# Optimization experiments

Measured on AMD Instinct MI355X. Metric: run time of the kernel, lower is better.

The kernel has to match this reference:

```python
import jax, jax.numpy as jnp
import numpy as np

BLOCK = 64      # block_size
NRAND = 3       # num_random_blocks
NUM_HEAD = 16
HEAD_DIM = 64
HIDDEN = 1024
PEN = -10000.0  # HF attn_mask_penalty


def _sparse_attn(q, k, v, band_mask, from_mask, to_mask, blocked_mask, rand_attn):
    # q,k,v: [B,H,S,D]; BigBird block-sparse attention (HF math).
    B, H, S, D = q.shape
    b, r = BLOCK, NRAND
    n = S // b
    rsd = 1.0 / (D ** 0.5)

    bq = q.reshape(B, H, n, b, D)
    bk = k.reshape(B, H, n, b, D)
    bv = v.reshape(B, H, n, b, D)

    bi = jnp.arange(B)[:, None, None, None]
    hi = jnp.arange(H)[None, :, None, None]
    # gathered random key/value blocks: [B,H,n-2,r*b,D]
    gk = bk[bi, hi, rand_attn].reshape(B, H, n - 2, r * b, D)
    gv = bv[bi, hi, rand_attn].reshape(B, H, n - 2, r * b, D)
    # random-block mask: [B,H,n-2,b,r*b]
    rm = blocked_mask[bi, rand_attn].reshape(B, H, n - 2, r * b)
    rand_mask = jnp.einsum("blq,bhlk->bhlqk", blocked_mask[:, 1:-1], rm)

    ones = lambda shp: jnp.ones(shp, q.dtype)

    # ---- first query block: attends to everything ----
    p = jnp.einsum("bhqd,bhkd->bhqk", bq[:, :, 0], k) * rsd + (1.0 - to_mask) * PEN
    c0 = jnp.einsum("bhqk,bhkd->bhqd", jax.nn.softmax(p, -1), v)[:, :, None]

    # ---- second query block: blocks 0,1,2,last + random ----
    k1 = jnp.concatenate([bk[:, :, 0], bk[:, :, 1], bk[:, :, 2], bk[:, :, -1], gk[:, :, 0]], axis=2)
    v1 = jnp.concatenate([bv[:, :, 0], bv[:, :, 1], bv[:, :, 2], bv[:, :, -1], gv[:, :, 0]], axis=2)
    p = jnp.einsum("bhqd,bhkd->bhqk", bq[:, :, 1], k1) * rsd
    seq_pad = jnp.concatenate([to_mask[..., :3 * b], to_mask[..., -b:], ones((B, 1, 1, r * b))], axis=3)
    rand_pad = jnp.concatenate([ones((B, H, b, 4 * b)), rand_mask[:, :, 0]], axis=3)
    p = p + (1.0 - jnp.minimum(seq_pad, rand_pad)) * PEN
    c1 = jnp.einsum("bhqk,bhkd->bhqd", jax.nn.softmax(p, -1), v1)[:, :, None]

    # ---- middle blocks 2..n-3: band(3 blocks) + first + last + random ----
    ek = jnp.concatenate([bk[:, :, 1:-3], bk[:, :, 2:-2], bk[:, :, 3:-1]], axis=3)  # [B,H,n-4,3b,D]
    ev = jnp.concatenate([bv[:, :, 1:-3], bv[:, :, 2:-2], bv[:, :, 3:-1]], axis=3)
    mq = bq[:, :, 2:-2]                                                              # [B,H,n-4,b,D]
    inner = jnp.einsum("bhlqd,bhlkd->bhlqk", mq, ek) * rsd + (1.0 - band_mask) * PEN
    randp = jnp.einsum("bhlqd,bhlkd->bhlqk", mq, gk[:, :, 1:-1]) * rsd + (1.0 - rand_mask[:, :, 1:-1]) * PEN
    firstp = jnp.einsum("bhlqd,bhkd->bhlqk", mq, bk[:, :, 0]) * rsd + (1.0 - to_mask[..., :b][:, :, None]) * PEN
    lastp = jnp.einsum("bhlqd,bhkd->bhlqk", mq, bk[:, :, -1]) * rsd + (1.0 - to_mask[..., -b:][:, :, None]) * PEN
    band = jnp.concatenate([firstp, inner, randp, lastp], axis=-1)  # [B,H,n-4,b,(5+r)*b]
    a = jax.nn.softmax(band, -1)
    cm = jnp.einsum("bhlqk,bhlkd->bhlqd", a[..., b:4 * b], ev)
    cm = cm + jnp.einsum("bhlqk,bhlkd->bhlqd", a[..., 4 * b:-b], gv[:, :, 1:-1])
    cm = cm + jnp.einsum("bhlqk,bhkd->bhlqd", a[..., :b], bv[:, :, 0])
    cm = cm + jnp.einsum("bhlqk,bhkd->bhlqd", a[..., -b:], bv[:, :, -1])

    # ---- second-last query block: blocks 0,-3,-2,-1 + random ----
    k2 = jnp.concatenate([bk[:, :, 0], bk[:, :, -3], bk[:, :, -2], bk[:, :, -1], gk[:, :, -1]], axis=2)
    v2 = jnp.concatenate([bv[:, :, 0], bv[:, :, -3], bv[:, :, -2], bv[:, :, -1], gv[:, :, -1]], axis=2)
    p = jnp.einsum("bhqd,bhkd->bhqk", bq[:, :, -2], k2) * rsd
    seq_pad = jnp.concatenate([to_mask[..., :b], to_mask[..., -3 * b:], ones((B, 1, 1, r * b))], axis=3)
    rand_pad = jnp.concatenate([ones((B, H, b, 4 * b)), rand_mask[:, :, -1]], axis=3)
    p = p + (1.0 - jnp.minimum(seq_pad, rand_pad)) * PEN
    c2 = jnp.einsum("bhqk,bhkd->bhqd", jax.nn.softmax(p, -1), v2)[:, :, None]

    # ---- last query block: attends to everything ----
    p = jnp.einsum("bhqd,bhkd->bhqk", bq[:, :, -1], k) * rsd + (1.0 - to_mask) * PEN
    c3 = jnp.einsum("bhqk,bhkd->bhqd", jax.nn.softmax(p, -1), v)[:, :, None]

    ctx = jnp.concatenate([c0, c1, cm, c2, c3], axis=2).reshape(B, H, S, D)
    ctx = ctx * from_mask  # [B,1,S,1]
    return ctx.transpose(0, 2, 1, 3).reshape(B, S, H * D)


def setup_inputs() -> dict:
    key = jax.random.key(0)
    ks = jax.random.split(key, 12)
    B, L = 2, 4064
    S = 4096
    n = S // BLOCK
    sc = 0.02
    inp = {
        "X": jax.random.normal(ks[0], (B, L, HIDDEN), jnp.float32),
        "Wq": jax.random.normal(ks[1], (HIDDEN, NUM_HEAD * HEAD_DIM), jnp.float32) * sc,
        "b_q": jnp.zeros((NUM_HEAD * HEAD_DIM,), jnp.float32),
        "Wk": jax.random.normal(ks[2], (HIDDEN, NUM_HEAD * HEAD_DIM), jnp.float32) * sc,
        "b_k": jnp.zeros((NUM_HEAD * HEAD_DIM,), jnp.float32),
        "Wv": jax.random.normal(ks[3], (HIDDEN, NUM_HEAD * HEAD_DIM), jnp.float32) * sc,
        "b_v": jnp.zeros((NUM_HEAD * HEAD_DIM,), jnp.float32),
        "Wo": jax.random.normal(ks[4], (NUM_HEAD * HEAD_DIM, HIDDEN), jnp.float32) * sc,
        "b_o": jnp.zeros((HIDDEN,), jnp.float32),
        "band_mask": jnp.ones((B, 1, n - 4, BLOCK, 3 * BLOCK), jnp.float32),
        "from_mask": jnp.ones((B, 1, S, 1), jnp.float32),
        "to_mask": jnp.ones((B, 1, 1, S), jnp.float32),
        "blocked_encoder_mask": jnp.ones((B, n, BLOCK), jnp.float32),
        "rand_attn": jax.random.randint(ks[5], (B, NUM_HEAD, n - 2, NRAND), 0, n, jnp.int32),
    }
    return inp


def reference(X, Wq, b_q, Wk, b_k, Wv, b_v, Wo, b_o,
              band_mask, from_mask, to_mask, blocked_encoder_mask, rand_attn):
    B, L, _ = X.shape
    pad = BLOCK - L % BLOCK  # matches torch wrapper (pads full block if L % b == 0)
    Xp = jnp.pad(X, ((0, 0), (0, pad), (0, 0)))
    S = L + pad

    def proj(W, bias):
        return (Xp @ W + bias).reshape(B, S, NUM_HEAD, HEAD_DIM).transpose(0, 2, 1, 3)

    q, k, v = proj(Wq, b_q), proj(Wk, b_k), proj(Wv, b_v)
    attn = _sparse_attn(q, k, v, band_mask, from_mask, to_mask, blocked_encoder_mask, rand_attn)
    out = attn @ Wo + b_o
    return out[:, :L]
```

## Files before the change

### kernel.cpp

```cpp
#include <hip/hip_runtime.h>

#define BB 2
#define SEQ 4096
#define LQ 4064
#define HID 1024
#define NH 16
#define HD 64
#define NB 64
#define BLK 64
#define NR 3
#define PENV -10000.0f

typedef __bf16 bf16;
typedef __bf16 bf16x8 __attribute__((ext_vector_type(8)));
typedef float floatx4 __attribute__((ext_vector_type(4)));

__device__ inline floatx4 mfma16(bf16x8 a, bf16x8 b, floatx4 c) {
    return __builtin_amdgcn_mfma_f32_16x16x32_bf16(a, b, c, 0, 0, 0);
}

__device__ inline void async_ld16(const bf16* g, bf16* l) {
    __builtin_amdgcn_global_load_lds(
        (const __attribute__((address_space(1))) unsigned int*)g,
        (__attribute__((address_space(3))) unsigned int*)l, 16, 0, 0);
}

__global__ __launch_bounds__(256) void cast_pad_x(const float* __restrict__ X,
                                                  bf16* __restrict__ Xp) {
    int t = blockIdx.x * 256 + threadIdx.x;
    int c4 = t & 255;
    int row = t >> 8;
    int b = row >> 12;
    int s = row & 4095;
    float4 v = make_float4(0.f, 0.f, 0.f, 0.f);
    if (s < LQ) {
        v = reinterpret_cast<const float4*>(X + ((size_t)(b * LQ + s)) * HID)[c4];
    }
    union { bf16 h[4]; uint2 u; } o;
    o.h[0] = (bf16)v.x; o.h[1] = (bf16)v.y; o.h[2] = (bf16)v.z; o.h[3] = (bf16)v.w;
    *reinterpret_cast<uint2*>(Xp + (size_t)row * HID + c4 * 4) = o.u;
}

__global__ __launch_bounds__(256) void transpose_w(const float* __restrict__ Wq,
                                                   const float* __restrict__ Wk,
                                                   const float* __restrict__ Wv,
                                                   const float* __restrict__ Wo,
                                                   bf16* __restrict__ WqkvT,
                                                   bf16* __restrict__ WoT) {
    __shared__ float tile[64][65];
    int sel = blockIdx.z;
    const float* src = (sel == 0) ? Wq : (sel == 1) ? Wk : (sel == 2) ? Wv : Wo;
    bf16* dst = (sel < 3) ? (WqkvT + (size_t)sel * HID * HID) : WoT;
    int j0 = blockIdx.x * 64, k0 = blockIdx.y * 64;
    int tx = threadIdx.x, ty = threadIdx.y;
    for (int i = 0; i < 16; i++) {
        int k = ty + i * 4;
        tile[k][tx] = src[(size_t)(k0 + k) * HID + j0 + tx];
    }
    __syncthreads();
    for (int i = 0; i < 16; i++) {
        int j = ty + i * 4;
        dst[(size_t)(j0 + j) * HID + k0 + tx] = (bf16)tile[tx][j];
    }
}

__global__ __launch_bounds__(256) void transpose_band(const float* __restrict__ band,
                                                      float* __restrict__ bandT) {
    __shared__ float tile[64][65];
    int kt = blockIdx.x;
    int lrow = blockIdx.y;
    int b = blockIdx.z;
    const float* src = band + ((size_t)(b * (NB - 4) + lrow) * BLK) * 192;
    float* dst = bandT + ((size_t)(b * (NB - 4) + lrow) * 192) * BLK;
    int tx = threadIdx.x, ty = threadIdx.y;
    for (int i = 0; i < 16; i++) {
        int qq = i * 4 + ty;
        tile[qq][tx] = src[(size_t)qq * 192 + kt * 64 + tx];
    }
    __syncthreads();
    for (int i = 0; i < 16; i++) {
        int k = i * 4 + ty;
        dst[(size_t)(kt * 64 + k) * BLK + tx] = tile[tx][k];
    }
}

__global__ __launch_bounds__(256) void gemm_qkv(const bf16* __restrict__ Xp,
                                                const bf16* __restrict__ WT,
                                                const float* __restrict__ bq,
                                                const float* __restrict__ bk,
                                                const float* __restrict__ bv,
                                                bf16* __restrict__ qo,
                                                bf16* __restrict__ ko,
                                                bf16* __restrict__ vt) {
    __shared__ __align__(16) bf16 As[128 * 64];
    __shared__ __align__(16) bf16 Bs[128 * 64];
    int tid = threadIdx.x;
    int wave = tid >> 6, lane = tid & 63;
    int quad = lane >> 4, lm = lane & 15;
    int tile_m = blockIdx.x * 128;
    int tile_n = blockIdx.y * 128;
    int wm = (wave & 1) * 64, wn = (wave >> 1) * 64;

    floatx4 acc[4][4] = {};

    for (int k0 = 0; k0 < HID; k0 += 64) {
        __syncthreads();
        for (int it = 0; it < 4; it++) {
            int c = it * 256 + tid;
            int row = c >> 3, col = (c & 7) * 8;
            async_ld16(Xp + (size_t)(tile_m + row) * HID + k0 + col, &As[c * 8]);
            async_ld16(WT + (size_t)(tile_n + row) * HID + k0 + col, &Bs[c * 8]);
        }
        __syncthreads();
        for (int ks = 0; ks < 64; ks += 32) {
            bf16x8 a[4], b[4];
            for (int i = 0; i < 4; i++)
                a[i] = *reinterpret_cast<const bf16x8*>(&As[(wm + i * 16 + lm) * 64 + ks + quad * 8]);
            for (int j = 0; j < 4; j++)
                b[j] = *reinterpret_cast<const bf16x8*>(&Bs[(wn + j * 16 + lm) * 64 + ks + quad * 8]);
            for (int i = 0; i < 4; i++)
                for (int j = 0; j < 4; j++)
                    acc[i][j] = mfma16(a[i], b[j], acc[i][j]);
        }
    }

    for (int i = 0; i < 4; i++) {
        for (int j = 0; j < 4; j++) {
            int nn = tile_n + wn + j * 16 + lm;
            int which = nn >> 10;
            int hc = nn & 1023;
            const float* bias = (which == 0) ? bq : (which == 1) ? bk : bv;
            float bsv = bias[hc];
            int h = hc >> 6, d = hc & 63;
            for (int r = 0; r < 4; r++) {
                int mm = tile_m + wm + i * 16 + quad * 4 + r;
                int b_ = mm >> 12, s = mm & 4095;
                float val = acc[i][j][r] + bsv;
                if (which == 0) {
                    qo[((size_t)((b_ * NH + h) * SEQ + s)) * HD + d] = (bf16)(val * 0.125f);
                } else if (which == 1) {
                    ko[((size_t)((b_ * NH + h) * SEQ + s)) * HD + d] = (bf16)val;
                } else {
                    vt[((size_t)((b_ * NH + h) * HD + d)) * SEQ + s] = (bf16)val;
                }
            }
        }
    }
}

__global__ __launch_bounds__(256, 2) void attn_kernel(const bf16* __restrict__ q,
                                                      const bf16* __restrict__ kk,
                                                      const bf16* __restrict__ vt,
                                                      const float* __restrict__ bandT,
                                                      const float* __restrict__ fromm,
                                                      const float* __restrict__ tom,
                                                      const float* __restrict__ blocked,
                                                      const int* __restrict__ rand_attn,
                                                      bf16* __restrict__ attn) {
    __shared__ __align__(16) char smem[33792 + 512];

    int tid = threadIdx.x, wave = tid >> 6, lane = tid & 63;
    int quad = lane >> 4, lm = lane & 15;
    int bh = blockIdx.x;
    int b = bh >> 4, h = bh & 15;
    size_t bh_base = (size_t)bh * SEQ * HD;
    int x = blockIdx.y;
    bool fullmode = (x < 8);
    int l, sub;
    if (fullmode) { l = (x >> 2) ? (NB - 1) : 0; sub = x & 3; }
    else          { l = x - 7;                   sub = wave;  }

    bf16x8 aq0 = *reinterpret_cast<const bf16x8*>(
        q + bh_base + (size_t)(l * BLK + sub * 16 + lm) * HD + quad * 8);
    bf16x8 aq1 = *reinterpret_cast<const bf16x8*>(
        q + bh_base + (size_t)(l * BLK + sub * 16 + lm) * HD + 32 + quad * 8);

    floatx4 ctx[4] = {};
    float mrun = -1e30f, lrun = 0.f;
    float mq = blocked[((size_t)b * NB + l) * BLK + sub * 16 + lm];

    int blist[8], btype[8];
    if (!fullmode) {
        int base;
        if (l == 1) {
            blist[0] = 0; blist[1] = 1; blist[2] = 2; blist[3] = NB - 1;
            btype[0] = btype[1] = btype[2] = btype[3] = 0;
            base = 4;
        } else if (l == NB - 2) {
            blist[0] = 0; blist[1] = NB - 3; blist[2] = NB - 2; blist[3] = NB - 1;
            btype[0] = btype[1] = btype[2] = btype[3] = 0;
            base = 4;
        } else {
            blist[0] = 0;      btype[0] = 0;
            blist[1] = l - 1;  btype[1] = 1;
            blist[2] = l;      btype[2] = 2;
            blist[3] = l + 1;  btype[3] = 3;
            blist[4] = NB - 1; btype[4] = 0;
            base = 5;
        }
        const int* ra = rand_attn + ((size_t)(b * NH + h) * (NB - 2) + (l - 1)) * NR;
        for (int r = 0; r < NR; r++) { blist[base + r] = ra[r]; btype[base + r] = 4; }
        for (int i = base + NR; i < 8; i++) { blist[i] = 0; btype[i] = 5; }
    }

    bf16* pw = (bf16*)smem + wave * 16 * 264;

    int nch = fullmode ? 4 : 2;
    for (int ch = 0; ch < nch; ch++) {
        floatx4 sc[4][4];
        #pragma unroll
        for (int ib = 0; ib < 4; ib++) {
            int kb  = fullmode ? (wave * 16 + ch * 4 + ib) : blist[ch * 4 + ib];
            int typ = fullmode ? 0 : btype[ch * 4 + ib];
            const bf16* kbase = kk + bh_base + (size_t)kb * BLK * HD;
            #pragma unroll
            for (int f = 0; f < 4; f++) {
                bf16x8 a0 = *reinterpret_cast<const bf16x8*>(kbase + (f * 16 + lm) * HD + quad * 8);
                bf16x8 a1 = *reinterpret_cast<const bf16x8*>(kbase + (f * 16 + lm) * HD + 32 + quad * 8);
                floatx4 z = {0.f, 0.f, 0.f, 0.f};
                z = mfma16(a0, aq0, z);
                z = mfma16(a1, aq1, z);
                sc[ib][f] = z;
            }
            if (typ == 0) {
                #pragma unroll
                for (int f = 0; f < 4; f++) {
                    float4 t4 = *reinterpret_cast<const float4*>(
                        tom + (size_t)b * SEQ + kb * BLK + f * 16 + quad * 4);
                    sc[ib][f][0] += (1.f - t4.x) * PENV;
                    sc[ib][f][1] += (1.f - t4.y) * PENV;
                    sc[ib][f][2] += (1.f - t4.z) * PENV;
                    sc[ib][f][3] += (1.f - t4.w) * PENV;
                }
            } else if (typ == 4) {
                #pragma unroll
                for (int f = 0; f < 4; f++) {
                    float4 t4 = *reinterpret_cast<const float4*>(
                        blocked + ((size_t)b * NB + kb) * BLK + f * 16 + quad * 4);
                    sc[ib][f][0] += (1.f - mq * t4.x) * PENV;
                    sc[ib][f][1] += (1.f - mq * t4.y) * PENV;
                    sc[ib][f][2] += (1.f - mq * t4.z) * PENV;
                    sc[ib][f][3] += (1.f - mq * t4.w) * PENV;
                }
            } else if (typ != 5) {
                int t = typ - 1;
                const float* bp = bandT + ((size_t)(b * (NB - 4) + (l - 2)) * 192 + t * 64) * BLK;
                #pragma unroll
                for (int f = 0; f < 4; f++)
                    #pragma unroll
                    for (int r = 0; r < 4; r++) {
                        float bm = bp[(size_t)(f * 16 + quad * 4 + r) * BLK + sub * 16 + lm];
                        sc[ib][f][r] += (1.f - bm) * PENV;
                    }
            } else {
                #pragma unroll
                for (int f = 0; f < 4; f++)
                    #pragma unroll
                    for (int r = 0; r < 4; r++) sc[ib][f][r] += PENV;
            }
        }

        float mx = -1e30f;
        #pragma unroll
        for (int ib = 0; ib < 4; ib++)
            #pragma unroll
            for (int f = 0; f < 4; f++)
                #pragma unroll
                for (int r = 0; r < 4; r++) mx = fmaxf(mx, sc[ib][f][r]);
        mx = fmaxf(mx, __shfl_xor(mx, 16, 64));
        mx = fmaxf(mx, __shfl_xor(mx, 32, 64));
        float mnew = fmaxf(mrun, mx);
        float scale = __expf(mrun - mnew);
        lrun *= scale;
        #pragma unroll
        for (int dj = 0; dj < 4; dj++) ctx[dj] *= scale;
        mrun = mnew;

        __builtin_amdgcn_wave_barrier();
        float rs = 0.f;
        #pragma unroll
        for (int ib = 0; ib < 4; ib++)
            #pragma unroll
            for (int f = 0; f < 4; f++) {
                float p0 = __expf(sc[ib][f][0] - mnew);
                float p1 = __expf(sc[ib][f][1] - mnew);
                float p2 = __expf(sc[ib][f][2] - mnew);
                float p3 = __expf(sc[ib][f][3] - mnew);
                rs += (p0 + p1) + (p2 + p3);
                union { bf16 hh[4]; uint2 u; } pu;
                pu.hh[0] = (bf16)p0; pu.hh[1] = (bf16)p1;
                pu.hh[2] = (bf16)p2; pu.hh[3] = (bf16)p3;
                *reinterpret_cast<uint2*>(pw + lm * 264 + ib * 64 + f * 16 + quad * 4) = pu.u;
            }
        __builtin_amdgcn_wave_barrier();
        rs += __shfl_xor(rs, 16, 64);
        rs += __shfl_xor(rs, 32, 64);
        lrun += rs;

        #pragma unroll
        for (int ib = 0; ib < 4; ib++) {
            int kb = fullmode ? (wave * 16 + ch * 4 + ib) : blist[ch * 4 + ib];
            const bf16* vtb = vt + (size_t)bh * HD * SEQ + (size_t)kb * BLK;
            bf16x8 pb0 = *reinterpret_cast<const bf16x8*>(pw + lm * 264 + ib * 64 + quad * 8);
            bf16x8 pb1 = *reinterpret_cast<const bf16x8*>(pw + lm * 264 + ib * 64 + 32 + quad * 8);
            #pragma unroll
            for (int dj = 0; dj < 4; dj++) {
                bf16x8 aV0 = *reinterpret_cast<const bf16x8*>(
                    vtb + (size_t)(dj * 16 + lm) * SEQ + quad * 8);
                bf16x8 aV1 = *reinterpret_cast<const bf16x8*>(
                    vtb + (size_t)(dj * 16 + lm) * SEQ + 32 + quad * 8);
                ctx[dj] = mfma16(aV0, pb0, ctx[dj]);
                ctx[dj] = mfma16(aV1, pb1, ctx[dj]);
            }
        }
    }

    if (!fullmode) {
        int sq = l * BLK + sub * 16 + lm;
        float w = (1.f / lrun) * fromm[(size_t)b * SEQ + sq];
        bf16* dst = attn + ((size_t)(b * SEQ + sq)) * HID + h * HD;
        #pragma unroll
        for (int dj = 0; dj < 4; dj++) {
            union { bf16 hh[4]; uint2 u; } o;
            #pragma unroll
            for (int r = 0; r < 4; r++) o.hh[r] = (bf16)(ctx[dj][r] * w);
            *reinterpret_cast<uint2*>(dst + dj * 16 + quad * 4) = o.u;
        }
    } else {
        float* ctxL = (float*)smem;
        float* mL   = (float*)(smem + 33792);
        float* lL   = (float*)(smem + 33792 + 256);
        __syncthreads();
        #pragma unroll
        for (int dj = 0; dj < 4; dj++)
            #pragma unroll
            for (int r = 0; r < 4; r++)
                ctxL[wave * 1024 + (dj * 16 + quad * 4 + r) * 16 + lm] = ctx[dj][r];
        if (quad == 0) { mL[wave * 16 + lm] = mrun; lL[wave * 16 + lm] = lrun; }
        __syncthreads();
        int qq = tid & 15, dbase = (tid >> 4) * 4;
        float M = -1e30f;
        for (int w = 0; w < 4; w++) M = fmaxf(M, mL[w * 16 + qq]);
        float e[4], Lt = 0.f;
        for (int w = 0; w < 4; w++) { e[w] = __expf(mL[w * 16 + qq] - M); Lt += lL[w * 16 + qq] * e[w]; }
        int sq = l * BLK + sub * 16 + qq;
        float wgt = (1.f / Lt) * fromm[(size_t)b * SEQ + sq];
        union { bf16 hh[4]; uint2 u; } o;
        #pragma unroll
        for (int dd = 0; dd < 4; dd++) {
            float acc = 0.f;
            for (int w = 0; w < 4; w++) acc += ctxL[w * 1024 + (dbase + dd) * 16 + qq] * e[w];
            o.hh[dd] = (bf16)(acc * wgt);
        }
        *reinterpret_cast<uint2*>(attn + ((size_t)(b * SEQ + sq)) * HID + h * HD + dbase) = o.u;
    }
}

__global__ __launch_bounds__(256) void gemm_out(const bf16* __restrict__ A,
                                                const bf16* __restrict__ WoT,
                                                const float* __restrict__ bo,
                                                float* __restrict__ out) {
    __shared__ __align__(16) bf16 As[128 * 64];
    __shared__ __align__(16) bf16 Bs[128 * 64];
    int tid = threadIdx.x;
    int wave = tid >> 6, lane = tid & 63;
    int quad = lane >> 4, lm = lane & 15;
    int tile_m = blockIdx.x * 128;
    int tile_n = blockIdx.y * 128;
    int wm = (wave & 1) * 64, wn = (wave >> 1) * 64;

    floatx4 acc[4][4] = {};

    for (int k0 = 0; k0 < HID; k0 += 64) {
        __syncthreads();
        for (int it = 0; it < 4; it++) {
            int c = it * 256 + tid;
            int row = c >> 3, col = (c & 7) * 8;
            async_ld16(A + (size_t)(tile_m + row) * HID + k0 + col, &As[c * 8]);
            async_ld16(WoT + (size_t)(tile_n + row) * HID + k0 + col, &Bs[c * 8]);
        }
        __syncthreads();
        for (int ks = 0; ks < 64; ks += 32) {
            bf16x8 a[4], b[4];
            for (int i = 0; i < 4; i++)
                a[i] = *reinterpret_cast<const bf16x8*>(&As[(wm + i * 16 + lm) * 64 + ks + quad * 8]);
            for (int j = 0; j < 4; j++)
                b[j] = *reinterpret_cast<const bf16x8*>(&Bs[(wn + j * 16 + lm) * 64 + ks + quad * 8]);
            for (int i = 0; i < 4; i++)
                for (int j = 0; j < 4; j++)
                    acc[i][j] = mfma16(a[i], b[j], acc[i][j]);
        }
    }

    for (int i = 0; i < 4; i++) {
        for (int j = 0; j < 4; j++) {
            int nn = tile_n + wn + j * 16 + lm;
            float bsv = bo[nn];
            for (int r = 0; r < 4; r++) {
                int mm = tile_m + wm + i * 16 + quad * 4 + r;
                int b_ = mm >> 12, s = mm & 4095;
                if (s < LQ)
                    out[((size_t)(b_ * LQ + s)) * HID + nn] = acc[i][j][r] + bsv;
            }
        }
    }
}

extern "C" void kernel_launch(void* const* d_in, const int* in_sizes, int n_in,
                              void* d_out, int out_size, void* d_ws, size_t ws_size,
                              hipStream_t stream) {
    const float* X       = (const float*)d_in[0];
    const float* Wq      = (const float*)d_in[1];
    const float* bq      = (const float*)d_in[2];
    const float* Wk      = (const float*)d_in[3];
    const float* bk      = (const float*)d_in[4];
    const float* Wv      = (const float*)d_in[5];
    const float* bv      = (const float*)d_in[6];
    const float* Wo      = (const float*)d_in[7];
    const float* bo      = (const float*)d_in[8];
    const float* band    = (const float*)d_in[9];
    const float* fromm   = (const float*)d_in[10];
    const float* tom     = (const float*)d_in[11];
    const float* blocked = (const float*)d_in[12];
    const int*   randa   = (const int*)d_in[13];
    float* out = (float*)d_out;

    char* ws = (char*)d_ws;
    bf16* Xp    = (bf16*)(ws + 0);
    bf16* WqkvT = (bf16*)(ws + 16777216);
    bf16* WoT   = (bf16*)(ws + 23068672);
    bf16* qb    = (bf16*)(ws + 25165824);
    bf16* kb    = (bf16*)(ws + 41943040);
    bf16* vtb   = (bf16*)(ws + 58720256);
    bf16* attnb = Xp;
    float* bandT = (float*)WqkvT;

    cast_pad_x<<<dim3(8192), dim3(256), 0, stream>>>(X, Xp);
    transpose_w<<<dim3(16, 16, 4), dim3(64, 4), 0, stream>>>(Wq, Wk, Wv, Wo, WqkvT, WoT);
    gemm_qkv<<<dim3(64, 24), dim3(256), 0, stream>>>(Xp, WqkvT, bq, bk, bv, qb, kb, vtb);
    transpose_band<<<dim3(3, NB - 4, BB), dim3(64, 4), 0, stream>>>(band, bandT);
    attn_kernel<<<dim3(BB * NH, 70), dim3(256), 0, stream>>>(qb, kb, vtb, bandT, fromm, tom,
                                                             blocked, randa, attnb);
    gemm_out<<<dim3(64, 8), dim3(256), 0, stream>>>(attnb, WoT, bo, out);
}
```

Before: 407.3 us.

## Stage QKV GEMM epilogue through LDS and remap tiles for XCD locality

The QKV GEMM epilogue now writes each wave's 64x64 output tile into padded shared memory, then emits contiguous 16-byte stores for q/k rows and for transposed v rows. This replaces scattered 2-byte global stores, especially the strided transposed v writes. Both GEMMs also switch to a 1D grid with a block-to-tile mapping that places neighbouring M tiles on the same XCD, aiming for better L2 reuse. The cost is extra LDS traffic and a barrier in the epilogue.

Result: faster. 398.2 us (-2.2%).

```diff
diff --git a/kernel.cpp b/kernel.cpp
--- a/kernel.cpp
+++ b/kernel.cpp
@@ -92,13 +92,16 @@
                                                 bf16* __restrict__ qo,
                                                 bf16* __restrict__ ko,
                                                 bf16* __restrict__ vt) {
-    __shared__ __align__(16) bf16 As[128 * 64];
-    __shared__ __align__(16) bf16 Bs[128 * 64];
+    __shared__ __align__(16) char smem[36864];
+    bf16* As = (bf16*)smem;
+    bf16* Bs = As + 128 * 64;
     int tid = threadIdx.x;
     int wave = tid >> 6, lane = tid & 63;
     int quad = lane >> 4, lm = lane & 15;
-    int tile_m = blockIdx.x * 128;
-    int tile_n = blockIdx.y * 128;
+    int id = blockIdx.x;
+    int xcd = id & 7, slot = id >> 3;
+    int tile_m = (xcd * 8 + (slot & 7)) * 128;
+    int tile_n = (slot >> 3) * 128;
     int wm = (wave & 1) * 64, wn = (wave >> 1) * 64;
 
     floatx4 acc[4][4] = {};
@@ -124,27 +127,54 @@
         }
     }
 
-    for (int i = 0; i < 4; i++) {
-        for (int j = 0; j < 4; j++) {
-            int nn = tile_n + wn + j * 16 + lm;
-            int which = nn >> 10;
-            int hc = nn & 1023;
-            const float* bias = (which == 0) ? bq : (which == 1) ? bk : bv;
-            float bsv = bias[hc];
-            int h = hc >> 6, d = hc & 63;
-            for (int r = 0; r < 4; r++) {
-                int mm = tile_m + wm + i * 16 + quad * 4 + r;
-                int b_ = mm >> 12, s = mm & 4095;
-                float val = acc[i][j][r] + bsv;
-                if (which == 0) {
-                    qo[((size_t)((b_ * NH + h) * SEQ + s)) * HD + d] = (bf16)(val * 0.125f);
-                } else if (which == 1) {
-                    ko[((size_t)((b_ * NH + h) * SEQ + s)) * HD + d] = (bf16)val;
-                } else {
-                    vt[((size_t)((b_ * NH + h) * HD + d)) * SEQ + s] = (bf16)val;
+    int which = tile_n >> 10;
+    int hc_base = (tile_n + wn) & 1023;
+    int h = hc_base >> 6;
+    const float* bias = (which == 0) ? bq : (which == 1) ? bk : bv;
+    __syncthreads();
+    bf16* ep = (bf16*)smem + wave * (64 * 72);
+
+    if (which < 2) {
+        #pragma unroll
+        for (int i = 0; i < 4; i++)
+            #pragma unroll
+            for (int j = 0; j < 4; j++) {
+                float bsv = bias[hc_base + j * 16 + lm];
+                #pragma unroll
+                for (int r = 0; r < 4; r++) {
+                    float val = acc[i][j][r] + bsv;
+                    if (which == 0) val *= 0.125f;
+                    ep[(i * 16 + quad * 4 + r) * 72 + j * 16 + lm] = (bf16)val;
                 }
             }
-        }
+        __builtin_amdgcn_wave_barrier();
+        int s_glob = tile_m + wm + lane;
+        int b_ = s_glob >> 12, s = s_glob & 4095;
+        bf16* dstb = ((which == 0) ? qo : ko) + ((size_t)((b_ * NH + h) * SEQ + s)) * HD;
+        #pragma unroll
+        for (int c = 0; c < 8; c++)
+            *reinterpret_cast<uint4*>(dstb + c * 8) =
+                *reinterpret_cast<const uint4*>(ep + lane * 72 + c * 8);
+    } else {
+        #pragma unroll
+        for (int i = 0; i < 4; i++)
+            #pragma unroll
+            for (int j = 0; j < 4; j++) {
+                float bsv = bias[hc_base + j * 16 + lm];
+                #pragma unroll
+                for (int r = 0; r < 4; r++) {
+                    float val = acc[i][j][r] + bsv;
+                    ep[(j * 16 + lm) * 72 + i * 16 + quad * 4 + r] = (bf16)val;
+                }
+            }
+        __builtin_amdgcn_wave_barrier();
+        int s_base = tile_m + wm;
+        int b_ = s_base >> 12, s0 = s_base & 4095;
+        bf16* dstb = vt + ((size_t)((b_ * NH + h) * HD + lane)) * SEQ + s0;
+        #pragma unroll
+        for (int c = 0; c < 8; c++)
+            *reinterpret_cast<uint4*>(dstb + c * 8) =
+                *reinterpret_cast<const uint4*>(ep + lane * 72 + c * 8);
     }
 }
 
@@ -365,8 +395,10 @@
     int tid = threadIdx.x;
     int wave = tid >> 6, lane = tid & 63;
     int quad = lane >> 4, lm = lane & 15;
-    int tile_m = blockIdx.x * 128;
-    int tile_n = blockIdx.y * 128;
+    int id = blockIdx.x;
+    int xcd = id & 7, slot = id >> 3;
+    int tile_m = (xcd * 8 + (slot & 7)) * 128;
+    int tile_n = (slot >> 3) * 128;
     int wm = (wave & 1) * 64, wn = (wave >> 1) * 64;
 
     floatx4 acc[4][4] = {};
@@ -437,9 +469,9 @@
 
     cast_pad_x<<<dim3(8192), dim3(256), 0, stream>>>(X, Xp);
     transpose_w<<<dim3(16, 16, 4), dim3(64, 4), 0, stream>>>(Wq, Wk, Wv, Wo, WqkvT, WoT);
-    gemm_qkv<<<dim3(64, 24), dim3(256), 0, stream>>>(Xp, WqkvT, bq, bk, bv, qb, kb, vtb);
+    gemm_qkv<<<dim3(1536), dim3(256), 0, stream>>>(Xp, WqkvT, bq, bk, bv, qb, kb, vtb);
     transpose_band<<<dim3(3, NB - 4, BB), dim3(64, 4), 0, stream>>>(band, bandT);
     attn_kernel<<<dim3(BB * NH, 70), dim3(256), 0, stream>>>(qb, kb, vtb, bandT, fromm, tom,
                                                              blocked, randa, attnb);
-    gemm_out<<<dim3(64, 8), dim3(256), 0, stream>>>(attnb, WoT, bo, out);
-}
+    gemm_out<<<dim3(512), dim3(256), 0, stream>>>(attnb, WoT, bo, out);
+}
```
